# Performance work log

Measured on AMD Instinct MI355X. Metric: run time of the kernel, lower is better.

Reference implementation:

```python
import jax, jax.numpy as jnp
import numpy as np

N_DATA = 40000   # max_training_points
D_PCA = 16       # n_pca_components
D_FEAT = 384     # raw feature dim
Q = 8192         # number of query points


def setup_inputs() -> dict:
    key = jax.random.key(0)
    k1, k2, k3, k4, k5 = jax.random.split(key, 5)
    features = jax.random.normal(k1, (Q, D_FEAT), dtype=jnp.float32)
    pca_mean = jax.random.normal(k2, (D_FEAT,), dtype=jnp.float32) * 0.1
    singular_vectors = jax.random.normal(k3, (D_FEAT, D_PCA), dtype=jnp.float32) / np.sqrt(D_FEAT)
    max_length = jnp.asarray(4.0, dtype=jnp.float32)  # max L2 norm seen at fit time
    # bw_transform is lower-triangular (Cholesky of scaled inverse covariance)
    bw = jax.random.normal(k4, (D_PCA, D_PCA), dtype=jnp.float32) * 0.2
    bw_transform = jnp.tril(bw) + 1.5 * jnp.eye(D_PCA, dtype=jnp.float32)
    dataset = jax.random.normal(k5, (N_DATA, D_PCA), dtype=jnp.float32)  # already bw-transformed at fit
    # norm = prod(diag(bw)) * (2*pi)^(-d/2)
    norm = jnp.prod(jnp.diag(bw_transform)) * jnp.asarray((2 * np.pi) ** (-D_PCA / 2), jnp.float32)
    return {
        'features': features,
        'pca_mean': pca_mean,
        'singular_vectors': singular_vectors,
        'max_length': max_length,
        'bw_transform': bw_transform,
        'dataset': dataset,
        'norm': norm,
    }


def reference(features, pca_mean, singular_vectors, max_length, bw_transform, dataset, norm):
    # PCA.transform: center then project
    f = jnp.matmul(features - pca_mean, singular_vectors)          # [Q, d]
    # pre_process with SCALE method
    f = f / max_length
    # GaussianKDE.forward: bandwidth transform then pairwise sq-dist to dataset
    f = jnp.matmul(f, bw_transform)                                # [Q, d]
    # ||dataset_j - f_i||^2 = |f|^2 + |ds|^2 - 2 f.ds  (vectorized, no QxNxd tensor)
    d2 = (jnp.sum(f * f, axis=1, keepdims=True)
          + jnp.sum(dataset * dataset, axis=1)[None, :]
          - 2.0 * jnp.matmul(f, dataset.T))                        # [Q, N]
    estimate = jnp.mean(jnp.exp(-0.5 * d2), axis=1) * norm         # [Q]
    scores = jnp.log(estimate + 1e-300)                            # log-likelihood
    # compute_probabilities
    return 1.0 / (1.0 + jnp.exp(0.05 * (scores - 12.0)))
```

## Files before the change

kernel.cpp:

```cpp
#include <hip/hip_runtime.h>
#include <hip/hip_bf16.h>

#define Q 8192
#define DF 384
#define DP 16
#define NDATA 40000
#define AUGK 32
#define QPRE_BLOCKS 512
#define DPRE_BLOCKS ((NDATA + 255) / 256)
#define NQBLK3 32
#define NCHUNK 64
#define SCH_C 126.95703125f
#define P23 8388608.f

typedef __attribute__((ext_vector_type(8))) short short8v;
typedef __attribute__((ext_vector_type(4))) float f32x4;

__device__ __forceinline__ unsigned short f2bf(float x) {
    union { float f; unsigned int u; } c; c.f = x;
    unsigned int u = c.u;
    u += 0x7fff + ((u >> 16) & 1);
    return (unsigned short)(u >> 16);
}
__device__ __forceinline__ float bf2f(unsigned short h) {
    union { float f; unsigned int u; } c; c.u = ((unsigned int)h) << 16;
    return c.f;
}
__device__ __forceinline__ float i2f_bits(int i) {
    union { int i; float f; } c; c.i = i; return c.f;
}
__device__ __forceinline__ float fexp2(float x) {
#if __has_builtin(__builtin_amdgcn_exp2f)
    return __builtin_amdgcn_exp2f(x);
#else
    float r; asm volatile("v_exp_f32 %0, %1" : "=v"(r) : "v"(x)); return r;
#endif
}

__global__ __launch_bounds__(384) void k_mm(
    const float* __restrict__ mean, const float* __restrict__ sv,
    const float* __restrict__ bw, const float* __restrict__ maxlen_p,
    float* __restrict__ M2, float* __restrict__ cc)
{
    __shared__ float bwl[256];
    __shared__ float red[384];
    __shared__ float cmps[16];
    int t = threadIdx.x;
    if (t < 256) bwl[t] = bw[t];
    {
        int k = t & 15, s = t >> 4;
        float a = 0.f;
        for (int d = s; d < DF; d += 24)
            a = fmaf(mean[d], sv[d * DP + k], a);
        red[t] = a;
    }
    __syncthreads();
    float scale = P23 * 1.4426950408889634f / (*maxlen_p);
    {
        const float4* s4 = (const float4*)(sv + (size_t)t * DP);
        float4 a0 = s4[0], a1 = s4[1], a2 = s4[2], a3 = s4[3];
        float svr[16] = {a0.x, a0.y, a0.z, a0.w, a1.x, a1.y, a1.z, a1.w,
                         a2.x, a2.y, a2.z, a2.w, a3.x, a3.y, a3.z, a3.w};
        float mrow[16];
#pragma unroll
        for (int j = 0; j < 16; ++j) {
            float m = 0.f;
#pragma unroll
            for (int k = 0; k < 16; ++k) m = fmaf(svr[k], bwl[k * 16 + j], m);
            mrow[j] = scale * m;
        }
        float4* md = (float4*)(M2 + (size_t)t * DP);
        md[0] = make_float4(mrow[0], mrow[1], mrow[2], mrow[3]);
        md[1] = make_float4(mrow[4], mrow[5], mrow[6], mrow[7]);
        md[2] = make_float4(mrow[8], mrow[9], mrow[10], mrow[11]);
        md[3] = make_float4(mrow[12], mrow[13], mrow[14], mrow[15]);
    }
    if (t < 16) {
        float m = 0.f;
        for (int s = 0; s < 24; ++s) m += red[s * 16 + t];
        cmps[t] = m;
    }
    __syncthreads();
    if (t < 16) {
        float s = 0.f;
#pragma unroll
        for (int k = 0; k < 16; ++k) s = fmaf(cmps[k], bwl[k * 16 + t], s);
        cc[t] = scale * s;
    }
}

__global__ __launch_bounds__(256) void k_pre(
    const float* __restrict__ feat, const float* __restrict__ ds,
    const float* __restrict__ M2, const float* __restrict__ cc,
    unsigned short* __restrict__ cfb, float* __restrict__ qb,
    unsigned short* __restrict__ dsb)
{
    int t = threadIdx.x;

    if (blockIdx.x >= QPRE_BLOCKS) {
        int j = (int)(blockIdx.x - QPRE_BLOCKS) * 256 + t;
        if (j < NDATA) {
            const float4* r = (const float4*)(ds + (size_t)j * DP);
            unsigned int pk[8];
            float ss = 0.f;
#pragma unroll
            for (int q4 = 0; q4 < 4; ++q4) {
                float4 v = r[q4];
                unsigned short h0 = f2bf(v.x), h1 = f2bf(v.y);
                unsigned short h2 = f2bf(v.z), h3 = f2bf(v.w);
                float f0 = bf2f(h0), f1 = bf2f(h1), f2 = bf2f(h2), f3 = bf2f(h3);
                ss += f0 * f0 + f1 * f1 + f2 * f2 + f3 * f3;
                pk[q4 * 2 + 0] = (unsigned int)h0 | ((unsigned int)h1 << 16);
                pk[q4 * 2 + 1] = (unsigned int)h2 | ((unsigned int)h3 << 16);
            }
            float v = fmaf(ss, -0.72134752044f, SCH_C);
            unsigned short hi = f2bf(v);
            unsigned short lo = f2bf(v - bf2f(hi));
            uint4* dst = (uint4*)(dsb + (size_t)j * AUGK);
            dst[0] = make_uint4(pk[0], pk[1], pk[2], pk[3]);
            dst[1] = make_uint4(pk[4], pk[5], pk[6], pk[7]);
            dst[2] = make_uint4((unsigned int)hi | ((unsigned int)lo << 16), 0u, 0u, 0u);
            dst[3] = make_uint4(0u, 0u, 0u, 0u);
        }
        return;
    }

    __shared__ __align__(16) float m2l[DF * 20];
    __shared__ float ccl[16];
    const float4* m2g = (const float4*)M2;
#pragma unroll
    for (int it = 0; it < 6; ++it) {
        int i = it * 256 + t;
        int d = i >> 2, qq = i & 3;
        *(float4*)(m2l + d * 20 + qq * 4) = m2g[i];
    }
    if (t < 16) ccl[t] = cc[t];
    __syncthreads();

    int r = t >> 4, s = t & 15;
    int row = (int)blockIdx.x * 16 + r;
    float acc[16];
#pragma unroll
    for (int k = 0; k < 16; ++k) acc[k] = 0.f;
    const float* fr = feat + (size_t)row * DF;
#pragma unroll 4
    for (int c = 0; c < 24; ++c) {
        int d = s + (c << 4);
        float fv = fr[d];
        const float4* mr = (const float4*)(m2l + d * 20);
        float4 m0 = mr[0], m1 = mr[1], m2 = mr[2], m3 = mr[3];
        acc[0]  = fmaf(fv, m0.x, acc[0]);  acc[1]  = fmaf(fv, m0.y, acc[1]);
        acc[2]  = fmaf(fv, m0.z, acc[2]);  acc[3]  = fmaf(fv, m0.w, acc[3]);
        acc[4]  = fmaf(fv, m1.x, acc[4]);  acc[5]  = fmaf(fv, m1.y, acc[5]);
        acc[6]  = fmaf(fv, m1.z, acc[6]);  acc[7]  = fmaf(fv, m1.w, acc[7]);
        acc[8]  = fmaf(fv, m2.x, acc[8]);  acc[9]  = fmaf(fv, m2.y, acc[9]);
        acc[10] = fmaf(fv, m2.z, acc[10]); acc[11] = fmaf(fv, m2.w, acc[11]);
        acc[12] = fmaf(fv, m3.x, acc[12]); acc[13] = fmaf(fv, m3.y, acc[13]);
        acc[14] = fmaf(fv, m3.z, acc[14]); acc[15] = fmaf(fv, m3.w, acc[15]);
    }
#pragma unroll
    for (int k = 0; k < 16; ++k) {
        acc[k] += __shfl_xor(acc[k], 1);
        acc[k] += __shfl_xor(acc[k], 2);
        acc[k] += __shfl_xor(acc[k], 4);
        acc[k] += __shfl_xor(acc[k], 8);
    }
    if (s == 0) {
        unsigned int pk[16];
        unsigned short h[16];
        float s2 = 0.f;
#pragma unroll
        for (int k = 0; k < 16; ++k) {
            float f = acc[k] - ccl[k];
            h[k] = f2bf(f);
            float fr2 = bf2f(h[k]) * (1.f / P23);
            s2 += fr2 * fr2;
        }
        qb[row] = -0.34657359028f * s2;
#pragma unroll
        for (int p = 0; p < 8; ++p)
            pk[p] = (unsigned int)h[2 * p] | ((unsigned int)h[2 * p + 1] << 16);
        pk[8] = 0x4B004B00u;
#pragma unroll
        for (int p = 9; p < 16; ++p) pk[p] = 0u;
        uint4* dst = (uint4*)(cfb + (size_t)row * AUGK);
        dst[0] = make_uint4(pk[0], pk[1], pk[2], pk[3]);
        dst[1] = make_uint4(pk[4], pk[5], pk[6], pk[7]);
        dst[2] = make_uint4(pk[8], pk[9], pk[10], pk[11]);
        dst[3] = make_uint4(pk[12], pk[13], pk[14], pk[15]);
    }
}

#define COMPT(bf)                                                             \
    {                                                                         \
        f32x4 d0 = __builtin_amdgcn_mfma_f32_16x16x32_bf16(a0, bf, z, 0, 0, 0); \
        f32x4 d1 = __builtin_amdgcn_mfma_f32_16x16x32_bf16(a1, bf, z, 0, 0, 0); \
        f32x4 d2 = __builtin_amdgcn_mfma_f32_16x16x32_bf16(a2, bf, z, 0, 0, 0); \
        f32x4 d3 = __builtin_amdgcn_mfma_f32_16x16x32_bf16(a3, bf, z, 0, 0, 0); \
        _Pragma("unroll")                                                     \
        for (int r = 0; r < 4; ++r) {                                         \
            sacc[0][r] += i2f_bits((int)d0[r]);                               \
            sacc[1][r] += i2f_bits((int)d1[r]);                               \
            sacc[2][r] += i2f_bits((int)d2[r]);                               \
            sacc[3][r] += i2f_bits((int)d3[r]);                               \
        }                                                                     \
    }

__global__ __launch_bounds__(256, 8) void k3_main(
    const unsigned short* __restrict__ cfb, const unsigned short* __restrict__ dsb,
    float* __restrict__ partial)
{
    int t = threadIdx.x;
    int qblk = (int)blockIdx.x & (NQBLK3 - 1);
    int c    = (int)blockIdx.x >> 5;
    int w = t >> 6, l = t & 63;
    int qbase = qblk * 256 + w * 64;
    int kg = l >> 4, col = l & 15;

    int start = c * 39 + min(c, 4);
    int ntile = 39 + (c < 4 ? 1 : 0);
    int j0 = start * 16;

    const short8v* ap = (const short8v*)(cfb + (size_t)(qbase + col) * AUGK + kg * 8);
    short8v a0 = ap[0];
    short8v a1 = ap[64];
    short8v a2 = ap[128];
    short8v a3 = ap[192];

    const short8v* bp = (const short8v*)(dsb + (size_t)(j0 + col) * AUGK + kg * 8);

    float sacc[4][4] = {{0.f,0.f,0.f,0.f},{0.f,0.f,0.f,0.f},
                        {0.f,0.f,0.f,0.f},{0.f,0.f,0.f,0.f}};
    f32x4 z = {0.f, 0.f, 0.f, 0.f};

    int npair = ntile >> 1;
    short8v bf0 = bp[0];
    short8v bf1 = bp[64];
    for (int p = 0; p + 1 < npair; ++p) {
        short8v n0 = bp[(size_t)(2 * p + 2) * 64];
        short8v n1 = bp[(size_t)(2 * p + 3) * 64];
        COMPT(bf0);
        COMPT(bf1);
        bf0 = n0; bf1 = n1;
    }
    COMPT(bf0);
    COMPT(bf1);
    if (ntile & 1) {
        short8v bl = bp[(size_t)(ntile - 1) * 64];
        COMPT(bl);
    }

#pragma unroll
    for (int o = 1; o < 16; o <<= 1)
#pragma unroll
        for (int tt = 0; tt < 4; ++tt)
#pragma unroll
            for (int r = 0; r < 4; ++r)
                sacc[tt][r] += __shfl_xor(sacc[tt][r], o);

    if (col == 0) {
        float* dst = partial + (size_t)c * Q + qbase;
#pragma unroll
        for (int tt = 0; tt < 4; ++tt)
#pragma unroll
            for (int r = 0; r < 4; ++r)
                dst[tt * 16 + kg * 4 + r] = sacc[tt][r];
    }
}

__global__ __launch_bounds__(256) void k4_final(
    const float* __restrict__ partial, const float* __restrict__ qb,
    const float* __restrict__ norm_p, float* __restrict__ out)
{
    __shared__ float l2[8][33];
    int t = threadIdx.x;
    int ql = t & 31, sl = t >> 5;
    int q = (int)blockIdx.x * 32 + ql;
    float a = 0.f;
    for (int cc = sl; cc < NCHUNK; cc += 8) a += partial[(size_t)cc * Q + q];
    l2[sl][ql] = a;
    __syncthreads();
    if (t < 32) {
        int qq = (int)blockIdx.x * 32 + t;
        float s = 0.f;
#pragma unroll
        for (int s8 = 0; s8 < 8; ++s8) s += l2[s8][t];
        float est = (*norm_p) * (1.0f / (float)NDATA) * fexp2(qb[qq]) * s;
        float score = logf(est + 1e-38f);
        out[qq] = 1.0f / (1.0f + expf(0.05f * (score - 12.0f)));
    }
}

extern "C" void kernel_launch(void* const* d_in, const int* in_sizes, int n_in,
                              void* d_out, int out_size, void* d_ws, size_t ws_size,
                              hipStream_t stream) {
    const float* features = (const float*)d_in[0];
    const float* pca_mean = (const float*)d_in[1];
    const float* sv       = (const float*)d_in[2];
    const float* maxlen   = (const float*)d_in[3];
    const float* bw       = (const float*)d_in[4];
    const float* dataset  = (const float*)d_in[5];
    const float* norm     = (const float*)d_in[6];
    float* out = (float*)d_out;

    char* ws = (char*)d_ws;
    unsigned short* cfb = (unsigned short*)(ws);
    unsigned short* dsb = (unsigned short*)(ws + 524288);
    float* qb = (float*)(ws + 524288 + 2560000);
    float* M2 = (float*)(ws + 524288 + 2560000 + 32768);
    float* cc = (float*)(ws + 524288 + 2560000 + 32768 + 24576);
    float* partial = (float*)(ws + 524288 + 2560000 + 32768 + 24576 + 256);

    k_mm<<<1, 384, 0, stream>>>(pca_mean, sv, bw, maxlen, M2, cc);
    k_pre<<<QPRE_BLOCKS + DPRE_BLOCKS, 256, 0, stream>>>(
        features, dataset, M2, cc, cfb, qb, dsb);
    k3_main<<<NQBLK3 * NCHUNK, 256, 0, stream>>>(cfb, dsb, partial);
    k4_final<<<Q / 32, 256, 0, stream>>>(partial, qb, norm, out);
}
```

Before: 118.2 us.

## Fold projection setup into k_pre and final reduction into k3 via last-block counter

Result: slower. 311.1 us (+163.1%).

```diff
diff --git a/kernel.cpp b/kernel.cpp
--- a/kernel.cpp
+++ b/kernel.cpp
@@ -36,68 +36,25 @@
     float r; asm volatile("v_exp_f32 %0, %1" : "=v"(r) : "v"(x)); return r;
 #endif
 }
-
-__global__ __launch_bounds__(384) void k_mm(
+__device__ __forceinline__ float flog2(float x) {
+#if __has_builtin(__builtin_amdgcn_logf)
+    return __builtin_amdgcn_logf(x);
+#else
+    float r; asm volatile("v_log_f32 %0, %1" : "=v"(r) : "v"(x)); return r;
+#endif
+}
+
+__global__ __launch_bounds__(256) void k_pre(
+    const float* __restrict__ feat, const float* __restrict__ ds,
     const float* __restrict__ mean, const float* __restrict__ sv,
     const float* __restrict__ bw, const float* __restrict__ maxlen_p,
-    float* __restrict__ M2, float* __restrict__ cc)
-{
-    __shared__ float bwl[256];
-    __shared__ float red[384];
-    __shared__ float cmps[16];
-    int t = threadIdx.x;
-    if (t < 256) bwl[t] = bw[t];
-    {
-        int k = t & 15, s = t >> 4;
-        float a = 0.f;
-        for (int d = s; d < DF; d += 24)
-            a = fmaf(mean[d], sv[d * DP + k], a);
-        red[t] = a;
-    }
-    __syncthreads();
-    float scale = P23 * 1.4426950408889634f / (*maxlen_p);
-    {
-        const float4* s4 = (const float4*)(sv + (size_t)t * DP);
-        float4 a0 = s4[0], a1 = s4[1], a2 = s4[2], a3 = s4[3];
-        float svr[16] = {a0.x, a0.y, a0.z, a0.w, a1.x, a1.y, a1.z, a1.w,
-                         a2.x, a2.y, a2.z, a2.w, a3.x, a3.y, a3.z, a3.w};
-        float mrow[16];
-#pragma unroll
-        for (int j = 0; j < 16; ++j) {
-            float m = 0.f;
-#pragma unroll
-            for (int k = 0; k < 16; ++k) m = fmaf(svr[k], bwl[k * 16 + j], m);
-            mrow[j] = scale * m;
-        }
-        float4* md = (float4*)(M2 + (size_t)t * DP);
-        md[0] = make_float4(mrow[0], mrow[1], mrow[2], mrow[3]);
-        md[1] = make_float4(mrow[4], mrow[5], mrow[6], mrow[7]);
-        md[2] = make_float4(mrow[8], mrow[9], mrow[10], mrow[11]);
-        md[3] = make_float4(mrow[12], mrow[13], mrow[14], mrow[15]);
-    }
-    if (t < 16) {
-        float m = 0.f;
-        for (int s = 0; s < 24; ++s) m += red[s * 16 + t];
-        cmps[t] = m;
-    }
-    __syncthreads();
-    if (t < 16) {
-        float s = 0.f;
-#pragma unroll
-        for (int k = 0; k < 16; ++k) s = fmaf(cmps[k], bwl[k * 16 + t], s);
-        cc[t] = scale * s;
-    }
-}
-
-__global__ __launch_bounds__(256) void k_pre(
-    const float* __restrict__ feat, const float* __restrict__ ds,
-    const float* __restrict__ M2, const float* __restrict__ cc,
     unsigned short* __restrict__ cfb, float* __restrict__ qb,
-    unsigned short* __restrict__ dsb)
+    unsigned short* __restrict__ dsb, int* __restrict__ cnt)
 {
     int t = threadIdx.x;
 
     if (blockIdx.x >= QPRE_BLOCKS) {
+        if (blockIdx.x == QPRE_BLOCKS && t < NQBLK3) cnt[t] = 0;
         int j = (int)(blockIdx.x - QPRE_BLOCKS) * 256 + t;
         if (j < NDATA) {
             const float4* r = (const float4*)(ds + (size_t)j * DP);
@@ -126,15 +83,48 @@
     }
 
     __shared__ __align__(16) float m2l[DF * 20];
+    __shared__ float bwl[256];
+    __shared__ float red[256];
+    __shared__ float cmps[16];
     __shared__ float ccl[16];
-    const float4* m2g = (const float4*)M2;
-#pragma unroll
-    for (int it = 0; it < 6; ++it) {
-        int i = it * 256 + t;
-        int d = i >> 2, qq = i & 3;
-        *(float4*)(m2l + d * 20 + qq * 4) = m2g[i];
-    }
-    if (t < 16) ccl[t] = cc[t];
+
+    bwl[t] = bw[t];
+    {
+        int k = t & 15, s = t >> 4;
+        float a = 0.f;
+        for (int d = s; d < DF; d += 16)
+            a = fmaf(mean[d], sv[d * DP + k], a);
+        red[t] = a;
+    }
+    __syncthreads();
+    float scale = P23 * 1.4426950408889634f / (*maxlen_p);
+    for (int d = t; d < DF; d += 256) {
+        const float4* s4 = (const float4*)(sv + (size_t)d * DP);
+        float4 a0 = s4[0], a1 = s4[1], a2 = s4[2], a3 = s4[3];
+        float svr[16] = {a0.x, a0.y, a0.z, a0.w, a1.x, a1.y, a1.z, a1.w,
+                         a2.x, a2.y, a2.z, a2.w, a3.x, a3.y, a3.z, a3.w};
+        float* md = m2l + d * 20;
+#pragma unroll
+        for (int j = 0; j < 16; ++j) {
+            float m = 0.f;
+#pragma unroll
+            for (int k = 0; k < 16; ++k) m = fmaf(svr[k], bwl[k * 16 + j], m);
+            md[j] = scale * m;
+        }
+    }
+    if (t < 16) {
+        float m = 0.f;
+#pragma unroll
+        for (int s = 0; s < 16; ++s) m += red[s * 16 + t];
+        cmps[t] = m;
+    }
+    __syncthreads();
+    if (t < 16) {
+        float s = 0.f;
+#pragma unroll
+        for (int k = 0; k < 16; ++k) s = fmaf(cmps[k], bwl[k * 16 + t], s);
+        ccl[t] = scale * s;
+    }
     __syncthreads();
 
     int r = t >> 4, s = t & 15;
@@ -208,8 +198,10 @@
 
 __global__ __launch_bounds__(256, 8) void k3_main(
     const unsigned short* __restrict__ cfb, const unsigned short* __restrict__ dsb,
-    float* __restrict__ partial)
+    const float* __restrict__ qb, const float* __restrict__ norm_p,
+    float* __restrict__ partial, int* __restrict__ cnt, float* __restrict__ out)
 {
+    __shared__ int lastf;
     int t = threadIdx.x;
     int qblk = (int)blockIdx.x & (NQBLK3 - 1);
     int c    = (int)blockIdx.x >> 5;
@@ -219,7 +211,6 @@
 
     int start = c * 39 + min(c, 4);
     int ntile = 39 + (c < 4 ? 1 : 0);
-    int j0 = start * 16;
 
     const short8v* ap = (const short8v*)(cfb + (size_t)(qbase + col) * AUGK + kg * 8);
     short8v a0 = ap[0];
@@ -227,7 +218,7 @@
     short8v a2 = ap[128];
     short8v a3 = ap[192];
 
-    const short8v* bp = (const short8v*)(dsb + (size_t)(j0 + col) * AUGK + kg * 8);
+    const short8v* bp = (const short8v*)(dsb + ((size_t)(start * 16 + col) * AUGK) + kg * 8);
 
     float sacc[4][4] = {{0.f,0.f,0.f,0.f},{0.f,0.f,0.f,0.f},
                         {0.f,0.f,0.f,0.f},{0.f,0.f,0.f,0.f}};
@@ -236,9 +227,11 @@
     int npair = ntile >> 1;
     short8v bf0 = bp[0];
     short8v bf1 = bp[64];
+    bp += 128;
     for (int p = 0; p + 1 < npair; ++p) {
-        short8v n0 = bp[(size_t)(2 * p + 2) * 64];
-        short8v n1 = bp[(size_t)(2 * p + 3) * 64];
+        short8v n0 = bp[0];
+        short8v n1 = bp[64];
+        bp += 128;
         COMPT(bf0);
         COMPT(bf1);
         bf0 = n0; bf1 = n1;
@@ -246,7 +239,7 @@
     COMPT(bf0);
     COMPT(bf1);
     if (ntile & 1) {
-        short8v bl = bp[(size_t)(ntile - 1) * 64];
+        short8v bl = bp[0];
         COMPT(bl);
     }
 
@@ -266,29 +259,25 @@
             for (int r = 0; r < 4; ++r)
                 dst[tt * 16 + kg * 4 + r] = sacc[tt][r];
     }
-}
-
-__global__ __launch_bounds__(256) void k4_final(
-    const float* __restrict__ partial, const float* __restrict__ qb,
-    const float* __restrict__ norm_p, float* __restrict__ out)
-{
-    __shared__ float l2[8][33];
-    int t = threadIdx.x;
-    int ql = t & 31, sl = t >> 5;
-    int q = (int)blockIdx.x * 32 + ql;
-    float a = 0.f;
-    for (int cc = sl; cc < NCHUNK; cc += 8) a += partial[(size_t)cc * Q + q];
-    l2[sl][ql] = a;
+
+    __threadfence();
+    if (t == 0) lastf = (atomicAdd(&cnt[qblk], 1) == NCHUNK - 1) ? 1 : 0;
     __syncthreads();
-    if (t < 32) {
-        int qq = (int)blockIdx.x * 32 + t;
-        float s = 0.f;
-#pragma unroll
-        for (int s8 = 0; s8 < 8; ++s8) s += l2[s8][t];
-        float est = (*norm_p) * (1.0f / (float)NDATA) * fexp2(qb[qq]) * s;
-        float score = logf(est + 1e-38f);
-        out[qq] = 1.0f / (1.0f + expf(0.05f * (score - 12.0f)));
-    }
+    if (!lastf) return;
+    __threadfence();
+
+    int q = qblk * 256 + t;
+    float s0 = 0.f, s1 = 0.f, s2 = 0.f, s3 = 0.f;
+    const float* pp = partial + q;
+    for (int cc = 0; cc < NCHUNK; cc += 4) {
+        s0 += __hip_atomic_load(pp + (size_t)(cc + 0) * Q, __ATOMIC_RELAXED, __HIP_MEMORY_SCOPE_AGENT);
+        s1 += __hip_atomic_load(pp + (size_t)(cc + 1) * Q, __ATOMIC_RELAXED, __HIP_MEMORY_SCOPE_AGENT);
+        s2 += __hip_atomic_load(pp + (size_t)(cc + 2) * Q, __ATOMIC_RELAXED, __HIP_MEMORY_SCOPE_AGENT);
+        s3 += __hip_atomic_load(pp + (size_t)(cc + 3) * Q, __ATOMIC_RELAXED, __HIP_MEMORY_SCOPE_AGENT);
+    }
+    float ssum = (s0 + s1) + (s2 + s3);
+    float l2e = flog2((*norm_p) * (1.0f / (float)NDATA)) + qb[q] + flog2(ssum);
+    out[q] = 1.0f / (1.0f + fexp2(fmaf(0.05f, l2e, -0.8656170245333781f)));
 }
 
 extern "C" void kernel_launch(void* const* d_in, const int* in_sizes, int n_in,
@@ -307,13 +296,10 @@
     unsigned short* cfb = (unsigned short*)(ws);
     unsigned short* dsb = (unsigned short*)(ws + 524288);
     float* qb = (float*)(ws + 524288 + 2560000);
-    float* M2 = (float*)(ws + 524288 + 2560000 + 32768);
-    float* cc = (float*)(ws + 524288 + 2560000 + 32768 + 24576);
-    float* partial = (float*)(ws + 524288 + 2560000 + 32768 + 24576 + 256);
-
-    k_mm<<<1, 384, 0, stream>>>(pca_mean, sv, bw, maxlen, M2, cc);
+    int* cnt = (int*)(ws + 524288 + 2560000 + 32768);
+    float* partial = (float*)(ws + 524288 + 2560000 + 32768 + 512);
+
     k_pre<<<QPRE_BLOCKS + DPRE_BLOCKS, 256, 0, stream>>>(
-        features, dataset, M2, cc, cfb, qb, dsb);
-    k3_main<<<NQBLK3 * NCHUNK, 256, 0, stream>>>(cfb, dsb, partial);
-    k4_final<<<Q / 32, 256, 0, stream>>>(partial, qb, norm, out);
-}
+        features, dataset, pca_mean, sv, bw, maxlen, cfb, qb, dsb, cnt);
+    k3_main<<<NQBLK3 * NCHUNK, 256, 0, stream>>>(cfb, dsb, qb, norm, partial, cnt, out);
+}
```

## Fold projection-matrix setup into preprocess and stage dataset tiles via LDS double-buffering

Applied to the files above, without the earlier changes.

Measured after the change: 323.8 us. +173.9%, slower.

```diff
diff --git a/kernel.cpp b/kernel.cpp
--- a/kernel.cpp
+++ b/kernel.cpp
@@ -36,62 +36,16 @@
     float r; asm volatile("v_exp_f32 %0, %1" : "=v"(r) : "v"(x)); return r;
 #endif
 }
-
-__global__ __launch_bounds__(384) void k_mm(
+__device__ __forceinline__ void stage16(const void* g, void* lds) {
+    __builtin_amdgcn_global_load_lds(
+        (const __attribute__((address_space(1))) unsigned int*)g,
+        (__attribute__((address_space(3))) unsigned int*)lds, 16, 0, 0);
+}
+
+__global__ __launch_bounds__(256) void k_pre(
+    const float* __restrict__ feat, const float* __restrict__ ds,
     const float* __restrict__ mean, const float* __restrict__ sv,
     const float* __restrict__ bw, const float* __restrict__ maxlen_p,
-    float* __restrict__ M2, float* __restrict__ cc)
-{
-    __shared__ float bwl[256];
-    __shared__ float red[384];
-    __shared__ float cmps[16];
-    int t = threadIdx.x;
-    if (t < 256) bwl[t] = bw[t];
-    {
-        int k = t & 15, s = t >> 4;
-        float a = 0.f;
-        for (int d = s; d < DF; d += 24)
-            a = fmaf(mean[d], sv[d * DP + k], a);
-        red[t] = a;
-    }
-    __syncthreads();
-    float scale = P23 * 1.4426950408889634f / (*maxlen_p);
-    {
-        const float4* s4 = (const float4*)(sv + (size_t)t * DP);
-        float4 a0 = s4[0], a1 = s4[1], a2 = s4[2], a3 = s4[3];
-        float svr[16] = {a0.x, a0.y, a0.z, a0.w, a1.x, a1.y, a1.z, a1.w,
-                         a2.x, a2.y, a2.z, a2.w, a3.x, a3.y, a3.z, a3.w};
-        float mrow[16];
-#pragma unroll
-        for (int j = 0; j < 16; ++j) {
-            float m = 0.f;
-#pragma unroll
-            for (int k = 0; k < 16; ++k) m = fmaf(svr[k], bwl[k * 16 + j], m);
-            mrow[j] = scale * m;
-        }
-        float4* md = (float4*)(M2 + (size_t)t * DP);
-        md[0] = make_float4(mrow[0], mrow[1], mrow[2], mrow[3]);
-        md[1] = make_float4(mrow[4], mrow[5], mrow[6], mrow[7]);
-        md[2] = make_float4(mrow[8], mrow[9], mrow[10], mrow[11]);
-        md[3] = make_float4(mrow[12], mrow[13], mrow[14], mrow[15]);
-    }
-    if (t < 16) {
-        float m = 0.f;
-        for (int s = 0; s < 24; ++s) m += red[s * 16 + t];
-        cmps[t] = m;
-    }
-    __syncthreads();
-    if (t < 16) {
-        float s = 0.f;
-#pragma unroll
-        for (int k = 0; k < 16; ++k) s = fmaf(cmps[k], bwl[k * 16 + t], s);
-        cc[t] = scale * s;
-    }
-}
-
-__global__ __launch_bounds__(256) void k_pre(
-    const float* __restrict__ feat, const float* __restrict__ ds,
-    const float* __restrict__ M2, const float* __restrict__ cc,
     unsigned short* __restrict__ cfb, float* __restrict__ qb,
     unsigned short* __restrict__ dsb)
 {
@@ -126,15 +80,48 @@
     }
 
     __shared__ __align__(16) float m2l[DF * 20];
+    __shared__ float bwl[256];
+    __shared__ float red[256];
+    __shared__ float cmps[16];
     __shared__ float ccl[16];
-    const float4* m2g = (const float4*)M2;
-#pragma unroll
-    for (int it = 0; it < 6; ++it) {
-        int i = it * 256 + t;
-        int d = i >> 2, qq = i & 3;
-        *(float4*)(m2l + d * 20 + qq * 4) = m2g[i];
-    }
-    if (t < 16) ccl[t] = cc[t];
+
+    bwl[t] = bw[t];
+    {
+        int k = t & 15, s = t >> 4;
+        float a = 0.f;
+        for (int d = s; d < DF; d += 16)
+            a = fmaf(mean[d], sv[d * DP + k], a);
+        red[t] = a;
+    }
+    __syncthreads();
+    float scale = P23 * 1.4426950408889634f / (*maxlen_p);
+    for (int d = t; d < DF; d += 256) {
+        const float4* s4 = (const float4*)(sv + (size_t)d * DP);
+        float4 a0 = s4[0], a1 = s4[1], a2 = s4[2], a3 = s4[3];
+        float svr[16] = {a0.x, a0.y, a0.z, a0.w, a1.x, a1.y, a1.z, a1.w,
+                         a2.x, a2.y, a2.z, a2.w, a3.x, a3.y, a3.z, a3.w};
+        float* md = m2l + d * 20;
+#pragma unroll
+        for (int j = 0; j < 16; ++j) {
+            float m = 0.f;
+#pragma unroll
+            for (int k = 0; k < 16; ++k) m = fmaf(svr[k], bwl[k * 16 + j], m);
+            md[j] = scale * m;
+        }
+    }
+    if (t < 16) {
+        float m = 0.f;
+#pragma unroll
+        for (int s = 0; s < 16; ++s) m += red[s * 16 + t];
+        cmps[t] = m;
+    }
+    __syncthreads();
+    if (t < 16) {
+        float s = 0.f;
+#pragma unroll
+        for (int k = 0; k < 16; ++k) s = fmaf(cmps[k], bwl[k * 16 + t], s);
+        ccl[t] = scale * s;
+    }
     __syncthreads();
 
     int r = t >> 4, s = t & 15;
@@ -210,6 +197,7 @@
     const unsigned short* __restrict__ cfb, const unsigned short* __restrict__ dsb,
     float* __restrict__ partial)
 {
+    __shared__ __align__(16) char sbuf[2][4096];
     int t = threadIdx.x;
     int qblk = (int)blockIdx.x & (NQBLK3 - 1);
     int c    = (int)blockIdx.x >> 5;
@@ -219,7 +207,6 @@
 
     int start = c * 39 + min(c, 4);
     int ntile = 39 + (c < 4 ? 1 : 0);
-    int j0 = start * 16;
 
     const short8v* ap = (const short8v*)(cfb + (size_t)(qbase + col) * AUGK + kg * 8);
     short8v a0 = ap[0];
@@ -227,27 +214,36 @@
     short8v a2 = ap[128];
     short8v a3 = ap[192];
 
-    const short8v* bp = (const short8v*)(dsb + (size_t)(j0 + col) * AUGK + kg * 8);
+    int srcoff = ((l >> 2) << 6) + (((l & 3) ^ ((l >> 3) & 3)) << 4);
+    const char* gbase = (const char*)dsb + (size_t)(start + w) * 1024 + srcoff;
+    int rdoff = (col << 6) + (((kg ^ (col >> 1)) & 3) << 4) + ((kg & ~3) << 4);
 
     float sacc[4][4] = {{0.f,0.f,0.f,0.f},{0.f,0.f,0.f,0.f},
                         {0.f,0.f,0.f,0.f},{0.f,0.f,0.f,0.f}};
     f32x4 z = {0.f, 0.f, 0.f, 0.f};
 
-    int npair = ntile >> 1;
-    short8v bf0 = bp[0];
-    short8v bf1 = bp[64];
-    for (int p = 0; p + 1 < npair; ++p) {
-        short8v n0 = bp[(size_t)(2 * p + 2) * 64];
-        short8v n1 = bp[(size_t)(2 * p + 3) * 64];
-        COMPT(bf0);
-        COMPT(bf1);
-        bf0 = n0; bf1 = n1;
-    }
-    COMPT(bf0);
-    COMPT(bf1);
-    if (ntile & 1) {
-        short8v bl = bp[(size_t)(ntile - 1) * 64];
-        COMPT(bl);
+    int ngrp = (ntile + 3) >> 2;
+    stage16(gbase, &sbuf[0][w * 1024]);
+    __syncthreads();
+
+    for (int g = 0; g < ngrp; ++g) {
+        if (g + 1 < ngrp)
+            stage16(gbase + (size_t)(g + 1) * 4096, &sbuf[(g + 1) & 1][w * 1024]);
+        const char* sb = sbuf[g & 1] + rdoff;
+        if (g + 1 < ngrp) {
+            short8v b0 = *(const short8v*)(sb);
+            short8v b1 = *(const short8v*)(sb + 1024);
+            short8v b2 = *(const short8v*)(sb + 2048);
+            short8v b3 = *(const short8v*)(sb + 3072);
+            COMPT(b0); COMPT(b1); COMPT(b2); COMPT(b3);
+        } else {
+            int rem = ntile - g * 4;
+            for (int tt = 0; tt < rem; ++tt) {
+                short8v bt = *(const short8v*)(sb + tt * 1024);
+                COMPT(bt);
+            }
+        }
+        __syncthreads();
     }
 
 #pragma unroll
@@ -306,14 +302,11 @@
     char* ws = (char*)d_ws;
     unsigned short* cfb = (unsigned short*)(ws);
     unsigned short* dsb = (unsigned short*)(ws + 524288);
-    float* qb = (float*)(ws + 524288 + 2560000);
-    float* M2 = (float*)(ws + 524288 + 2560000 + 32768);
-    float* cc = (float*)(ws + 524288 + 2560000 + 32768 + 24576);
-    float* partial = (float*)(ws + 524288 + 2560000 + 32768 + 24576 + 256);
-
-    k_mm<<<1, 384, 0, stream>>>(pca_mean, sv, bw, maxlen, M2, cc);
+    float* qb = (float*)(ws + 524288 + 2560000 + 4096);
+    float* partial = (float*)(ws + 524288 + 2560000 + 4096 + 32768);
+
     k_pre<<<QPRE_BLOCKS + DPRE_BLOCKS, 256, 0, stream>>>(
-        features, dataset, M2, cc, cfb, qb, dsb);
+        features, dataset, pca_mean, sv, bw, maxlen, cfb, qb, dsb);
     k3_main<<<NQBLK3 * NCHUNK, 256, 0, stream>>>(cfb, dsb, partial);
     k4_final<<<Q / 32, 256, 0, stream>>>(partial, qb, norm, out);
 }
```
